# Kernel optimization log

Measured on AMD Instinct MI355X. Metric: run time of the kernel, lower is better.

The kernel has to match this reference:

```python
import jax, jax.numpy as jnp
import numpy as np

HIDDEN = 128
HEADS = 8
HEAD_DIM = HIDDEN // HEADS
N = 2048
SCALE = HEAD_DIM ** -0.5


def setup_inputs() -> dict:
    key = jax.random.key(0)
    ks = jax.random.split(key, 12)
    # xavier_uniform bound for square (HIDDEN, HIDDEN) weights
    bound = float(np.sqrt(6.0 / (HIDDEN + HIDDEN)))
    def w(k):
        return jax.random.uniform(k, (HIDDEN, HIDDEN), jnp.float32, -bound, bound)
    return {
        "x": jax.random.normal(ks[0], (N, HIDDEN), jnp.float32),
        "attention_bias": jax.random.normal(ks[1], (N, N, HEADS), jnp.float32),
        "key_padding_mask": jnp.zeros((N,), jnp.bool_),
        "Wq": w(ks[2]), "bq": jnp.zeros((HIDDEN,), jnp.float32),
        "Wk": w(ks[3]), "bk": jnp.zeros((HIDDEN,), jnp.float32),
        "Wv": w(ks[4]), "bv": jnp.zeros((HIDDEN,), jnp.float32),
        "Wo": w(ks[5]), "bo": jnp.zeros((HIDDEN,), jnp.float32),
    }


def reference(x, attention_bias, key_padding_mask, Wq, bq, Wk, bk, Wv, bv, Wo, bo):
    n = x.shape[0]
    # torch Linear: y = x @ W.T + b
    q = (x @ Wq.T + bq).reshape(n, HEADS, HEAD_DIM).transpose(1, 0, 2)  # (H, N, D)
    k = (x @ Wk.T + bk).reshape(n, HEADS, HEAD_DIM).transpose(1, 0, 2)
    v = (x @ Wv.T + bv).reshape(n, HEADS, HEAD_DIM).transpose(1, 0, 2)
    scores = jnp.einsum('hnd,hmd->hnm', q, k) * SCALE        # (H, N, N)
    scores = scores + attention_bias.transpose(2, 0, 1)       # additive graph bias
    mask = key_padding_mask[None, None, :]                    # (1, 1, N) over keys
    scores = jnp.where(mask, -jnp.inf, scores)
    attn = jax.nn.softmax(scores, axis=-1)
    out = jnp.einsum('hnm,hmd->hnd', attn, v)                 # (H, N, D)
    out = out.transpose(1, 0, 2).reshape(n, HIDDEN)
    return out @ Wo.T + bo
```

## Files before the change

kernel.cpp:

```cpp
#include <hip/hip_runtime.h>
#include <hip/hip_bf16.h>

#define NSEQ 2048
#define HID 128
#define HEADS 8
#define HD 16
#define SCALE 0.25f
#define TQ 16
#define TK 64
#define SPLIT 8
#define KT_PER (NSEQ / TK / SPLIT)
#define QROW 160
#define PM_W 36
#define PH_W (16 * PM_W + 4)

typedef unsigned short ushort_t;
typedef __attribute__((ext_vector_type(8))) short short8;
typedef __attribute__((ext_vector_type(4))) float floatx4;

__device__ __forceinline__ void unpack2(unsigned u, float& a, float& b) {
    union { unsigned x; float f; } lo, hi;
    lo.x = u << 16; hi.x = u & 0xffff0000u;
    a = lo.f; b = hi.f;
}
__device__ __forceinline__ void unpack8(uint4 u, float* f) {
    unpack2(u.x, f[0], f[1]); unpack2(u.y, f[2], f[3]);
    unpack2(u.z, f[4], f[5]); unpack2(u.w, f[6], f[7]);
}
__device__ __forceinline__ unsigned pack_bf16x2(float a, float b) {
    __hip_bfloat16 ba = __float2bfloat16(a);
    __hip_bfloat16 bb = __float2bfloat16(b);
    return (unsigned)*(ushort_t*)&ba | ((unsigned)*(ushort_t*)&bb << 16);
}

__global__ void transpose_kernel(const float* __restrict__ Wq, const float* __restrict__ Wk,
                                 const float* __restrict__ Wv, const float* __restrict__ Wo,
                                 float* __restrict__ wt)
{
    int idx = blockIdx.x * 256 + threadIdx.x;
    int w = idx >> 14, rem = idx & 16383;
    int row = rem >> 7, col = rem & 127;
    const float* W = (w == 0) ? Wq : (w == 1) ? Wk : (w == 2) ? Wv : Wo;
    wt[w * 16384 + col * HID + row] = W[rem];
}

__global__ __launch_bounds__(128) void qkv_kernel(
    const float* __restrict__ x, const float* __restrict__ WqT,
    const float* __restrict__ WkT, const float* __restrict__ WvT,
    const float* __restrict__ bq, const float* __restrict__ bk,
    const float* __restrict__ bv, float* __restrict__ Qm,
    __hip_bfloat16* __restrict__ Kb, __hip_bfloat16* __restrict__ Vt)
{
    __shared__ float xs[8 * HID];
    const int j = threadIdx.x;
    const int mat = blockIdx.x >> 8;
    const int rb = blockIdx.x & 255;
    const int r0 = rb * 8;
    const float* WT = (mat == 0) ? WqT : (mat == 1) ? WkT : WvT;
    const float* bb = (mat == 0) ? bq : (mat == 1) ? bk : bv;
    const float4* xg = (const float4*)(x + (size_t)r0 * HID);
    float4* xl = (float4*)xs;
    for (int i = j; i < 8 * HID / 4; i += 128) xl[i] = xg[i];
    __syncthreads();
    float acc[8];
#pragma unroll
    for (int r = 0; r < 8; ++r) acc[r] = 0.f;
#pragma unroll 4
    for (int i = 0; i < HID; ++i) {
        float w = WT[i * HID + j];
#pragma unroll
        for (int r = 0; r < 8; ++r) acc[r] = fmaf(xs[r * HID + i], w, acc[r]);
    }
    float bv_ = bb[j];
#pragma unroll
    for (int r = 0; r < 8; ++r) acc[r] += bv_;
    if (mat == 0) {
#pragma unroll
        for (int r = 0; r < 8; ++r) Qm[(size_t)(r0 + r) * HID + j] = acc[r];
    } else if (mat == 1) {
#pragma unroll
        for (int r = 0; r < 8; ++r) Kb[(size_t)(r0 + r) * HID + j] = __float2bfloat16(acc[r]);
    } else {
        unsigned u[4];
#pragma unroll
        for (int p = 0; p < 4; ++p) u[p] = pack_bf16x2(acc[2 * p], acc[2 * p + 1]);
        *(uint4*)((ushort_t*)Vt + (size_t)j * NSEQ + r0) = make_uint4(u[0], u[1], u[2], u[3]);
    }
}

__global__ __launch_bounds__(256, 4) void attn_kernel(
    const float* __restrict__ Qm, const __hip_bfloat16* __restrict__ Kb,
    const __hip_bfloat16* __restrict__ Vt, const float* __restrict__ bias,
    const unsigned char* __restrict__ mask, float* __restrict__ Op,
    float* __restrict__ Lp)
{
    __shared__ float qs[TQ * QROW];
    __shared__ float Pbuf[8 * PH_W];
    __shared__ float wl[4 * TQ * HEADS];

    const int t = threadIdx.x;
    const int lane = t & 63;
    const int wid = t >> 6;
    const int qb = blockIdx.x & 127;
    const int sp = blockIdx.x >> 7;
    const int n0 = qb * TQ;

    const int sc_mp = t >> 3;
    const int sc_h  = t & 7;
    const int kk = wid & 1;
    const int hbase = (wid >> 1) * 4;
    const int frag_m = lane & 15;
    const int frag_q = lane >> 4;

    {
        for (int idx = t; idx < 512; idx += 256) {
            int r = idx >> 5, c = idx & 31;
            int h = c >> 2, dg = c & 3;
            float4 v = ((const float4*)(Qm + (size_t)n0 * HID))[idx];
            *(float4*)&qs[r * QROW + h * 20 + dg * 4] = v;
        }
    }
    floatx4 acc[4];
#pragma unroll
    for (int hh = 0; hh < 4; ++hh) acc[hh] = (floatx4){0.f, 0.f, 0.f, 0.f};
    float lsum[TQ];
#pragma unroll
    for (int r = 0; r < TQ; ++r) lsum[r] = 0.0f;
    __syncthreads();

    for (int kt = 0; kt < KT_PER; ++kt) {
        const int m0 = (sp * KT_PER + kt) * TK;
        {
            const int m1 = m0 + sc_mp * 2;
            const ushort_t* kp = (const ushort_t*)Kb + (size_t)m1 * HID + sc_h * HD;
            uint4 ka = *(const uint4*)kp;
            uint4 kb2 = *(const uint4*)(kp + 8);
            uint4 kc = *(const uint4*)(kp + HID);
            uint4 kd = *(const uint4*)(kp + HID + 8);
            float k0[16], k1[16];
            unpack8(ka, k0); unpack8(kb2, k0 + 8);
            unpack8(kc, k1); unpack8(kd, k1 + 8);
            const bool msk0 = mask[m1] != 0;
            const bool msk1 = mask[m1 + 1] != 0;
            unsigned* Pw = (unsigned*)Pbuf;
#pragma unroll
            for (int rg = 0; rg < 2; ++rg) {
                float bb0[8], bb1[8];
                const float* bp = bias + (((size_t)(n0 + rg * 8)) * NSEQ + m1) * HEADS + sc_h;
#pragma unroll
                for (int rr = 0; rr < 8; ++rr) {
                    bb0[rr] = __builtin_nontemporal_load(bp + (size_t)rr * (NSEQ * HEADS));
                    bb1[rr] = __builtin_nontemporal_load(bp + (size_t)rr * (NSEQ * HEADS) + HEADS);
                }
#pragma unroll
                for (int rr = 0; rr < 8; ++rr) {
                    const int r = rg * 8 + rr;
                    const float* qr = &qs[r * QROW + sc_h * 20];
                    float qf[16];
                    *(float4*)&qf[0]  = *(const float4*)(qr);
                    *(float4*)&qf[4]  = *(const float4*)(qr + 4);
                    *(float4*)&qf[8]  = *(const float4*)(qr + 8);
                    *(float4*)&qf[12] = *(const float4*)(qr + 12);
                    float d0 = 0.f, d1 = 0.f;
#pragma unroll
                    for (int i = 0; i < 16; ++i) {
                        d0 = fmaf(qf[i], k0[i], d0);
                        d1 = fmaf(qf[i], k1[i], d1);
                    }
                    float s0 = fmaf(d0, SCALE, bb0[rr]);
                    float s1 = fmaf(d1, SCALE, bb1[rr]);
                    if (msk0) s0 = -INFINITY;
                    if (msk1) s1 = -INFINITY;
                    float e0 = __expf(s0);
                    float e1 = __expf(s1);
                    lsum[r] += e0 + e1;
                    Pw[sc_h * PH_W + r * PM_W + sc_mp] = pack_bf16x2(e0, e1);
                }
            }
        }
        __syncthreads();
        {
            const unsigned* Pw = (const unsigned*)Pbuf;
#pragma unroll
            for (int hh = 0; hh < 4; ++hh) {
                const int h = hbase + hh;
                const ushort_t* vrow = (const ushort_t*)Vt +
                    ((size_t)(h * HD + frag_m)) * NSEQ + m0 + kk * 32 + frag_q * 8;
                short8 bfrag = *(const short8*)vrow;
                short8 afrag = *(const short8*)&Pw[h * PH_W + frag_m * PM_W + kk * 16 + frag_q * 4];
                acc[hh] = __builtin_amdgcn_mfma_f32_16x16x32_bf16(afrag, bfrag, acc[hh], 0, 0, 0);
            }
        }
        __syncthreads();
    }

#pragma unroll
    for (int r = 0; r < TQ; ++r) {
        lsum[r] += __shfl_xor(lsum[r], 8);
        lsum[r] += __shfl_xor(lsum[r], 16);
        lsum[r] += __shfl_xor(lsum[r], 32);
    }
    if (lane < 8) {
#pragma unroll
        for (int r = 0; r < TQ; ++r)
            wl[wid * (TQ * HEADS) + r * 8 + lane] = lsum[r];
    }
    {
        float* obuf = Pbuf;
#pragma unroll
        for (int hh = 0; hh < 4; ++hh) {
#pragma unroll
            for (int reg = 0; reg < 4; ++reg) {
                int m = frag_q * 4 + reg;
                obuf[kk * 2048 + (hbase + hh) * 256 + m * 16 + frag_m] = acc[hh][reg];
            }
        }
    }
    __syncthreads();
    if (t < 128) {
        const float* obuf = Pbuf;
#pragma unroll
        for (int r = 0; r < TQ; ++r) {
            int h = t >> 4, d = t & 15;
            float v = obuf[h * 256 + r * 16 + d] + obuf[2048 + h * 256 + r * 16 + d];
            Op[((size_t)sp * NSEQ + n0 + r) * HID + t] = v;
        }
        const int r2 = t >> 3, h2 = t & 7;
        float l = wl[r2 * 8 + h2] + wl[128 + r2 * 8 + h2] +
                  wl[256 + r2 * 8 + h2] + wl[384 + r2 * 8 + h2];
        Lp[((size_t)sp * NSEQ + n0 + r2) * HEADS + h2] = l;
    }
}

__global__ __launch_bounds__(128) void proj_kernel(
    const float* __restrict__ Op, const float* __restrict__ Lp,
    const float* __restrict__ WoT, const float* __restrict__ bo,
    float* __restrict__ out)
{
    __shared__ float xs[4 * HID];
    const int j = threadIdx.x;
    const int r0 = blockIdx.x * 4;
    const int hh = j >> 4;
#pragma unroll
    for (int r = 0; r < 4; ++r) {
        const size_t n = r0 + r;
        float s = 0.f, l = 0.f;
#pragma unroll
        for (int sp = 0; sp < SPLIT; ++sp) {
            s += Op[((size_t)sp * NSEQ + n) * HID + j];
            l += Lp[((size_t)sp * NSEQ + n) * HEADS + hh];
        }
        xs[r * HID + j] = s / l;
    }
    __syncthreads();
    float acc[4];
#pragma unroll
    for (int r = 0; r < 4; ++r) acc[r] = 0.f;
#pragma unroll 4
    for (int i = 0; i < HID; ++i) {
        float w = WoT[i * HID + j];
#pragma unroll
        for (int r = 0; r < 4; ++r) acc[r] = fmaf(xs[r * HID + i], w, acc[r]);
    }
    float b = bo[j];
#pragma unroll
    for (int r = 0; r < 4; ++r)
        out[(size_t)(r0 + r) * HID + j] = acc[r] + b;
}

extern "C" void kernel_launch(void* const* d_in, const int* in_sizes, int n_in,
                              void* d_out, int out_size, void* d_ws, size_t ws_size,
                              hipStream_t stream) {
    const float* x    = (const float*)d_in[0];
    const float* bias = (const float*)d_in[1];
    const unsigned char* mask = (const unsigned char*)d_in[2];
    const float* Wq = (const float*)d_in[3];
    const float* bq = (const float*)d_in[4];
    const float* Wk = (const float*)d_in[5];
    const float* bk = (const float*)d_in[6];
    const float* Wv = (const float*)d_in[7];
    const float* bv = (const float*)d_in[8];
    const float* Wo = (const float*)d_in[9];
    const float* bo = (const float*)d_in[10];
    float* out = (float*)d_out;

    float* w = (float*)d_ws;
    float* WqT = w;
    float* WkT = w + 16384;
    float* WvT = w + 32768;
    float* WoT = w + 49152;
    float* Qm  = w + 65536;
    __hip_bfloat16* Kb = (__hip_bfloat16*)(w + 327680);
    __hip_bfloat16* Vt = (__hip_bfloat16*)(w + 458752);
    float* Op  = w + 589824;
    float* Lp  = w + 589824 + (size_t)SPLIT * NSEQ * HID;

    transpose_kernel<<<256, 256, 0, stream>>>(Wq, Wk, Wv, Wo, w);
    qkv_kernel<<<768, 128, 0, stream>>>(x, WqT, WkT, WvT, bq, bk, bv, Qm, Kb, Vt);
    attn_kernel<<<128 * SPLIT, 256, 0, stream>>>(Qm, Kb, Vt, bias, mask, Op, Lp);
    proj_kernel<<<512, 128, 0, stream>>>(Op, Lp, WoT, bo, out);
}
```

Measured before the change: 242.9 us.

## Tile weight transpose, shrink qkv/proj row blocks, hoist all bias loads

The weight transpose now goes through a shared-memory tile so both its reads and writes are coalesced. The qkv and projection kernels process fewer rows per block and launch more blocks, to spread work over more compute units. In the attention kernel, all 16 rows of bias are loaded up front with ordinary loads instead of two groups of nontemporal loads, so more memory requests are in flight at once. The cost is higher register pressure in the attention kernel and the loss of the nontemporal cache hint on the large bias stream.

```diff
diff --git a/kernel.cpp b/kernel.cpp
--- a/kernel.cpp
+++ b/kernel.cpp
@@ -33,15 +33,25 @@
     return (unsigned)*(ushort_t*)&ba | ((unsigned)*(ushort_t*)&bb << 16);
 }
 
-__global__ void transpose_kernel(const float* __restrict__ Wq, const float* __restrict__ Wk,
-                                 const float* __restrict__ Wv, const float* __restrict__ Wo,
-                                 float* __restrict__ wt)
+__global__ __launch_bounds__(256) void transpose_kernel(
+    const float* __restrict__ Wq, const float* __restrict__ Wk,
+    const float* __restrict__ Wv, const float* __restrict__ Wo,
+    float* __restrict__ wt)
 {
-    int idx = blockIdx.x * 256 + threadIdx.x;
-    int w = idx >> 14, rem = idx & 16383;
-    int row = rem >> 7, col = rem & 127;
-    const float* W = (w == 0) ? Wq : (w == 1) ? Wk : (w == 2) ? Wv : Wo;
-    wt[w * 16384 + col * HID + row] = W[rem];
+    __shared__ float ts[32][33];
+    const int mat = blockIdx.x >> 4, tile = blockIdx.x & 15;
+    const int r0 = (tile >> 2) * 32, c0 = (tile & 3) * 32;
+    const float* W = (mat == 0) ? Wq : (mat == 1) ? Wk : (mat == 2) ? Wv : Wo;
+    const int lr = threadIdx.x >> 5;
+    const int lc = threadIdx.x & 31;
+#pragma unroll
+    for (int i = 0; i < 4; ++i)
+        ts[lr + i * 8][lc] = W[(r0 + lr + i * 8) * HID + c0 + lc];
+    __syncthreads();
+    float* dst = wt + mat * 16384;
+#pragma unroll
+    for (int i = 0; i < 4; ++i)
+        dst[(c0 + lr + i * 8) * HID + r0 + lc] = ts[lc][lr + i * 8];
 }
 
 __global__ __launch_bounds__(128) void qkv_kernel(
@@ -51,40 +61,37 @@
     const float* __restrict__ bv, float* __restrict__ Qm,
     __hip_bfloat16* __restrict__ Kb, __hip_bfloat16* __restrict__ Vt)
 {
-    __shared__ float xs[8 * HID];
+    __shared__ float xs[4 * HID];
     const int j = threadIdx.x;
-    const int mat = blockIdx.x >> 8;
-    const int rb = blockIdx.x & 255;
-    const int r0 = rb * 8;
+    const int mat = blockIdx.x >> 9;
+    const int rb = blockIdx.x & 511;
+    const int r0 = rb * 4;
     const float* WT = (mat == 0) ? WqT : (mat == 1) ? WkT : WvT;
     const float* bb = (mat == 0) ? bq : (mat == 1) ? bk : bv;
-    const float4* xg = (const float4*)(x + (size_t)r0 * HID);
-    float4* xl = (float4*)xs;
-    for (int i = j; i < 8 * HID / 4; i += 128) xl[i] = xg[i];
-    __syncthreads();
-    float acc[8];
-#pragma unroll
-    for (int r = 0; r < 8; ++r) acc[r] = 0.f;
-#pragma unroll 4
+    ((float4*)xs)[j] = ((const float4*)(x + (size_t)r0 * HID))[j];
+    __syncthreads();
+    float acc[4];
+#pragma unroll
+    for (int r = 0; r < 4; ++r) acc[r] = 0.f;
+#pragma unroll 8
     for (int i = 0; i < HID; ++i) {
         float w = WT[i * HID + j];
 #pragma unroll
-        for (int r = 0; r < 8; ++r) acc[r] = fmaf(xs[r * HID + i], w, acc[r]);
+        for (int r = 0; r < 4; ++r) acc[r] = fmaf(xs[r * HID + i], w, acc[r]);
     }
     float bv_ = bb[j];
 #pragma unroll
-    for (int r = 0; r < 8; ++r) acc[r] += bv_;
+    for (int r = 0; r < 4; ++r) acc[r] += bv_;
     if (mat == 0) {
 #pragma unroll
-        for (int r = 0; r < 8; ++r) Qm[(size_t)(r0 + r) * HID + j] = acc[r];
+        for (int r = 0; r < 4; ++r) Qm[(size_t)(r0 + r) * HID + j] = acc[r];
     } else if (mat == 1) {
 #pragma unroll
-        for (int r = 0; r < 8; ++r) Kb[(size_t)(r0 + r) * HID + j] = __float2bfloat16(acc[r]);
+        for (int r = 0; r < 4; ++r) Kb[(size_t)(r0 + r) * HID + j] = __float2bfloat16(acc[r]);
     } else {
-        unsigned u[4];
-#pragma unroll
-        for (int p = 0; p < 4; ++p) u[p] = pack_bf16x2(acc[2 * p], acc[2 * p + 1]);
-        *(uint4*)((ushort_t*)Vt + (size_t)j * NSEQ + r0) = make_uint4(u[0], u[1], u[2], u[3]);
+        unsigned u0 = pack_bf16x2(acc[0], acc[1]);
+        unsigned u1 = pack_bf16x2(acc[2], acc[3]);
+        *(uint2*)((ushort_t*)Vt + (size_t)j * NSEQ + r0) = make_uint2(u0, u1);
     }
 }
 
@@ -132,6 +139,13 @@
         const int m0 = (sp * KT_PER + kt) * TK;
         {
             const int m1 = m0 + sc_mp * 2;
+            float bb0[TQ], bb1[TQ];
+            const float* bp = bias + ((size_t)n0 * NSEQ + m1) * HEADS + sc_h;
+#pragma unroll
+            for (int r = 0; r < TQ; ++r) {
+                bb0[r] = bp[(size_t)r * (NSEQ * HEADS)];
+                bb1[r] = bp[(size_t)r * (NSEQ * HEADS) + HEADS];
+            }
             const ushort_t* kp = (const ushort_t*)Kb + (size_t)m1 * HID + sc_h * HD;
             uint4 ka = *(const uint4*)kp;
             uint4 kb2 = *(const uint4*)(kp + 8);
@@ -144,38 +158,27 @@
             const bool msk1 = mask[m1 + 1] != 0;
             unsigned* Pw = (unsigned*)Pbuf;
 #pragma unroll
-            for (int rg = 0; rg < 2; ++rg) {
-                float bb0[8], bb1[8];
-                const float* bp = bias + (((size_t)(n0 + rg * 8)) * NSEQ + m1) * HEADS + sc_h;
-#pragma unroll
-                for (int rr = 0; rr < 8; ++rr) {
-                    bb0[rr] = __builtin_nontemporal_load(bp + (size_t)rr * (NSEQ * HEADS));
-                    bb1[rr] = __builtin_nontemporal_load(bp + (size_t)rr * (NSEQ * HEADS) + HEADS);
+            for (int r = 0; r < TQ; ++r) {
+                const float* qr = &qs[r * QROW + sc_h * 20];
+                float qf[16];
+                *(float4*)&qf[0]  = *(const float4*)(qr);
+                *(float4*)&qf[4]  = *(const float4*)(qr + 4);
+                *(float4*)&qf[8]  = *(const float4*)(qr + 8);
+                *(float4*)&qf[12] = *(const float4*)(qr + 12);
+                float d0 = 0.f, d1 = 0.f;
+#pragma unroll
+                for (int i = 0; i < 16; ++i) {
+                    d0 = fmaf(qf[i], k0[i], d0);
+                    d1 = fmaf(qf[i], k1[i], d1);
                 }
-#pragma unroll
-                for (int rr = 0; rr < 8; ++rr) {
-                    const int r = rg * 8 + rr;
-                    const float* qr = &qs[r * QROW + sc_h * 20];
-                    float qf[16];
-                    *(float4*)&qf[0]  = *(const float4*)(qr);
-                    *(float4*)&qf[4]  = *(const float4*)(qr + 4);
-                    *(float4*)&qf[8]  = *(const float4*)(qr + 8);
-                    *(float4*)&qf[12] = *(const float4*)(qr + 12);
-                    float d0 = 0.f, d1 = 0.f;
-#pragma unroll
-                    for (int i = 0; i < 16; ++i) {
-                        d0 = fmaf(qf[i], k0[i], d0);
-                        d1 = fmaf(qf[i], k1[i], d1);
-                    }
-                    float s0 = fmaf(d0, SCALE, bb0[rr]);
-                    float s1 = fmaf(d1, SCALE, bb1[rr]);
-                    if (msk0) s0 = -INFINITY;
-                    if (msk1) s1 = -INFINITY;
-                    float e0 = __expf(s0);
-                    float e1 = __expf(s1);
-                    lsum[r] += e0 + e1;
-                    Pw[sc_h * PH_W + r * PM_W + sc_mp] = pack_bf16x2(e0, e1);
-                }
+                float s0 = fmaf(d0, SCALE, bb0[r]);
+                float s1 = fmaf(d1, SCALE, bb1[r]);
+                if (msk0) s0 = -INFINITY;
+                if (msk1) s1 = -INFINITY;
+                float e0 = __expf(s0);
+                float e1 = __expf(s1);
+                lsum[r] += e0 + e1;
+                Pw[sc_h * PH_W + r * PM_W + sc_mp] = pack_bf16x2(e0, e1);
             }
         }
         __syncthreads();
@@ -237,12 +240,12 @@
     const float* __restrict__ WoT, const float* __restrict__ bo,
     float* __restrict__ out)
 {
-    __shared__ float xs[4 * HID];
+    __shared__ float xs[2 * HID];
     const int j = threadIdx.x;
-    const int r0 = blockIdx.x * 4;
+    const int r0 = blockIdx.x * 2;
     const int hh = j >> 4;
 #pragma unroll
-    for (int r = 0; r < 4; ++r) {
+    for (int r = 0; r < 2; ++r) {
         const size_t n = r0 + r;
         float s = 0.f, l = 0.f;
 #pragma unroll
@@ -253,19 +256,17 @@
         xs[r * HID + j] = s / l;
     }
     __syncthreads();
-    float acc[4];
-#pragma unroll
-    for (int r = 0; r < 4; ++r) acc[r] = 0.f;
-#pragma unroll 4
+    float acc[2];
+    acc[0] = 0.f; acc[1] = 0.f;
+#pragma unroll 8
     for (int i = 0; i < HID; ++i) {
         float w = WoT[i * HID + j];
-#pragma unroll
-        for (int r = 0; r < 4; ++r) acc[r] = fmaf(xs[r * HID + i], w, acc[r]);
+        acc[0] = fmaf(xs[i], w, acc[0]);
+        acc[1] = fmaf(xs[HID + i], w, acc[1]);
     }
     float b = bo[j];
-#pragma unroll
-    for (int r = 0; r < 4; ++r)
-        out[(size_t)(r0 + r) * HID + j] = acc[r] + b;
+    out[(size_t)r0 * HID + j] = acc[0] + b;
+    out[(size_t)(r0 + 1) * HID + j] = acc[1] + b;
 }
 
 extern "C" void kernel_launch(void* const* d_in, const int* in_sizes, int n_in,
@@ -295,8 +296,8 @@
     float* Op  = w + 589824;
     float* Lp  = w + 589824 + (size_t)SPLIT * NSEQ * HID;
 
-    transpose_kernel<<<256, 256, 0, stream>>>(Wq, Wk, Wv, Wo, w);
-    qkv_kernel<<<768, 128, 0, stream>>>(x, WqT, WkT, WvT, bq, bk, bv, Qm, Kb, Vt);
+    transpose_kernel<<<64, 256, 0, stream>>>(Wq, Wk, Wv, Wo, w);
+    qkv_kernel<<<1536, 128, 0, stream>>>(x, WqT, WkT, WvT, bq, bk, bv, Qm, Kb, Vt);
     attn_kernel<<<128 * SPLIT, 256, 0, stream>>>(Qm, Kb, Vt, bias, mask, Op, Lp);
-    proj_kernel<<<512, 128, 0, stream>>>(Op, Lp, WoT, bo, out);
-}
+    proj_kernel<<<1024, 128, 0, stream>>>(Op, Lp, WoT, bo, out);
+}
```

Result: slower. 251.6 us (+3.6%).
